# Kernel optimization log

Hardware: AMD Instinct MI355X
Metric: run time of the kernel (lower is better)

## Reference

```python
import jax, jax.numpy as jnp
import numpy as np

N = 100000
E = 640000
WIDTH = 128
NUM_FEATURES = 64


def _linear_relu(h, W, b):
    # LinearBlock with batch_norm=False, dropout=0.0 -> Linear + ReLU
    return jax.nn.relu(h @ W + b)


def setup_inputs() -> dict:
    key = jax.random.key(0)
    k = jax.random.split(key, 8)
    x = jax.random.normal(k[0], (N, WIDTH), dtype=jnp.float32)
    e = jax.random.randint(k[1], (2, E), 0, N, dtype=jnp.int32)
    e_feat = jax.random.normal(k[2], (E, NUM_FEATURES), dtype=jnp.float32)
    s_e = 1.0 / np.sqrt(WIDTH + NUM_FEATURES)
    s_m = 1.0 / np.sqrt(2 * WIDTH)
    W_edge = jax.random.uniform(k[3], (WIDTH + NUM_FEATURES, WIDTH), jnp.float32, -s_e, s_e)
    b_edge = jax.random.uniform(k[4], (WIDTH,), jnp.float32, -s_e, s_e)
    W_mlp = jax.random.uniform(k[5], (2 * WIDTH, WIDTH), jnp.float32, -s_m, s_m)
    b_mlp = jax.random.uniform(k[6], (WIDTH,), jnp.float32, -s_m, s_m)
    return {"x": x, "e": e, "e_feat": e_feat, "W_edge": W_edge, "b_edge": b_edge,
            "W_mlp": W_mlp, "b_mlp": b_mlp}


def reference(x, e, e_feat, W_edge, b_edge, W_mlp, b_mlp):
    src, dst = e[0], e[1]
    diffs = x[dst] - x[src]                                   # [E, width]
    ef = diffs + _linear_relu(jnp.concatenate([diffs, e_feat], axis=1), W_edge, b_edge)
    maxes = jax.ops.segment_max(ef, dst, num_segments=x.shape[0])  # [N, width]
    # torch_scatter.scatter_max leaves empty segments at 0
    maxes = jnp.where(jnp.isneginf(maxes), 0.0, maxes)
    return x + _linear_relu(jnp.concatenate([x, maxes], axis=1), W_mlp, b_mlp)
```

## Files before the change

### kernel.cpp

```cpp
#include <hip/hip_runtime.h>
#include <hip/hip_bf16.h>
#include <limits.h>

#define NNODES 100000
#define NEDGES 640000
#define WIDTH  128
#define NFEAT  64
#define KA     192
#define KA_PAD 200
#define KB     256
#define KB_PAD 264
#define MT     64
#define ST     130
#define NB_SCAN ((NNODES + 255) / 256)

typedef __attribute__((ext_vector_type(8))) short short8;
typedef __attribute__((ext_vector_type(4))) short short4v;
typedef __attribute__((ext_vector_type(4))) float floatx4;

__device__ __forceinline__ short f2bf_rne(float f) {
    unsigned u = __float_as_uint(f);
    unsigned r = u + 0x7fffu + ((u >> 16) & 1u);
    return (short)(r >> 16);
}
__device__ __forceinline__ short f2bf_t(float f) {
    return (short)(__float_as_uint(f) >> 16);
}
__device__ __forceinline__ float bf2f(short s) {
    return __uint_as_float(((unsigned)(unsigned short)s) << 16);
}
__device__ __forceinline__ unsigned encu(float f) {
    unsigned u = __float_as_uint(f);
    return (u & 0x80000000u) ? ~u : (u | 0x80000000u);
}
__device__ __forceinline__ float decu(unsigned e) {
    unsigned u = (e & 0x80000000u) ? (e ^ 0x80000000u) : ~e;
    return __uint_as_float(u);
}

__global__ __launch_bounds__(256) void prep_kernel(
    const float* __restrict__ W_edge, const float* __restrict__ W_mlp,
    short* __restrict__ We_t, short* __restrict__ Wm_t)
{
    int t = blockIdx.x * 256 + threadIdx.x;
    if (t < KA * WIDTH) {
        int k = t / WIDTH, n = t % WIDTH;
        We_t[n * KA + k] = f2bf_rne(W_edge[t]);
    } else if (t < (KA + KB) * WIDTH) {
        int j = t - KA * WIDTH;
        int k = j / WIDTH, n = j % WIDTH;
        Wm_t[n * KB + k] = f2bf_rne(W_mlp[j]);
    }
}

__global__ __launch_bounds__(256) void hist_kernel(
    const int* __restrict__ e, int* __restrict__ counts)
{
    int i = blockIdx.x * 256 + threadIdx.x;
    if (i < NEDGES) atomicAdd(&counts[e[NEDGES + i]], 1);
}

__global__ __launch_bounds__(256) void scanA_kernel(
    const int* __restrict__ counts, int* __restrict__ cursor, int* __restrict__ blockSum)
{
    __shared__ int s[256];
    int tid = threadIdx.x;
    int n = blockIdx.x * 256 + tid;
    int c = (n < NNODES) ? counts[n] : 0;
    s[tid] = c;
    __syncthreads();
    for (int off = 1; off < 256; off <<= 1) {
        int v = (tid >= off) ? s[tid - off] : 0;
        __syncthreads();
        s[tid] += v;
        __syncthreads();
    }
    if (n < NNODES) cursor[n] = s[tid] - c;
    if (tid == 255) blockSum[blockIdx.x] = s[255];
}

__global__ __launch_bounds__(512) void scanB_kernel(int* __restrict__ blockSum,
                                                    int* __restrict__ blockOff)
{
    __shared__ int s[512];
    int tid = threadIdx.x;
    int c = (tid < NB_SCAN) ? blockSum[tid] : 0;
    s[tid] = c;
    __syncthreads();
    for (int off = 1; off < 512; off <<= 1) {
        int v = (tid >= off) ? s[tid - off] : 0;
        __syncthreads();
        s[tid] += v;
        __syncthreads();
    }
    if (tid < NB_SCAN) blockOff[tid] = s[tid] - c;
}

__global__ __launch_bounds__(256) void scatter_kernel(
    const int* __restrict__ e, int* __restrict__ cursor,
    const int* __restrict__ blockOff,
    uint2* __restrict__ pSD, int* __restrict__ pEid)
{
    int i = blockIdx.x * 256 + threadIdx.x;
    if (i < NEDGES) {
        int s = e[i];
        int d = e[NEDGES + i];
        int p = atomicAdd(&cursor[d], 1) + blockOff[d >> 8];
        pSD[p] = make_uint2((unsigned)s, (unsigned)d);
        pEid[p] = i;
    }
}

__global__ __launch_bounds__(256, 4) void edge_kernel(
    const float* __restrict__ x, const float* __restrict__ e_feat,
    const short* __restrict__ We_t, const float* __restrict__ b_edge,
    const uint2* __restrict__ pSD, const int* __restrict__ pEid,
    unsigned* __restrict__ mEnc)
{
    __shared__ short sA[MT * KA_PAD];
    __shared__ float sBias[WIDTH];
    __shared__ int   sDst[MT];
    __shared__ int   sHeadRow[MT + 1];
    __shared__ int   sMeta[3];

    const int tid = threadIdx.x;
    if (tid < WIDTH) sBias[tid] = b_edge[tid];

    const int e0 = blockIdx.x * MT;
    const float4* xf4 = (const float4*)x;
    const float4* ef4 = (const float4*)e_feat;

    {
        int mq = tid >> 5, c = tid & 31;
        uint2 sd[8];
        #pragma unroll
        for (int j = 0; j < 8; ++j) sd[j] = pSD[e0 + mq + 8 * j];
        #pragma unroll
        for (int j = 0; j < 8; ++j) {
            int mm = mq + 8 * j;
            float4 xs = xf4[(size_t)sd[j].x * 32 + c];
            float4 xd = xf4[(size_t)sd[j].y * 32 + c];
            short4v df;
            df.x = f2bf_t(xd.x - xs.x);
            df.y = f2bf_t(xd.y - xs.y);
            df.z = f2bf_t(xd.z - xs.z);
            df.w = f2bf_t(xd.w - xs.w);
            *(short4v*)&sA[mm * KA_PAD + c * 4] = df;
            if (c == 0) sDst[mm] = (int)sd[j].y;
        }
        int mq2 = tid >> 4, c2 = tid & 15;
        int eid[4];
        #pragma unroll
        for (int j = 0; j < 4; ++j) eid[j] = pEid[e0 + mq2 + 16 * j];
        #pragma unroll
        for (int j = 0; j < 4; ++j) {
            int mm = mq2 + 16 * j;
            float4 fv = ef4[(size_t)eid[j] * 16 + c2];
            short4v sv;
            sv.x = f2bf_t(fv.x); sv.y = f2bf_t(fv.y);
            sv.z = f2bf_t(fv.z); sv.w = f2bf_t(fv.w);
            *(short4v*)&sA[mm * KA_PAD + WIDTH + c2 * 4] = sv;
        }
    }
    __syncthreads();

    if (tid < 64) {
        bool head = (tid == 0) || (sDst[tid] != sDst[tid - 1]);
        unsigned long long mask = __ballot(head);
        int rank = __popcll(mask & ((1ull << tid) - 1ull));
        if (head) sHeadRow[rank] = tid;
        if (tid == 0) {
            int nh = (int)__popcll(mask);
            sMeta[0] = nh;
            sHeadRow[nh] = MT;
            int prevSame = 0, nextSame = 0;
            if (e0 > 0)           prevSame = (pSD[e0 - 1].y  == (unsigned)sDst[0]);
            if (e0 + MT < NEDGES) nextSame = (pSD[e0 + MT].y == (unsigned)sDst[MT - 1]);
            sMeta[1] = prevSame; sMeta[2] = nextSame;
        }
    }

    const int wave = tid >> 6;
    const int lane = tid & 63;
    const int l15  = lane & 15;
    const int kq   = (lane >> 4) << 3;
    const int quad = lane >> 4;

    floatx4 acc[4][2];
    #pragma unroll
    for (int rt = 0; rt < 4; ++rt)
        #pragma unroll
        for (int ct = 0; ct < 2; ++ct)
            acc[rt][ct] = (floatx4){0.f, 0.f, 0.f, 0.f};

    #pragma unroll
    for (int kc = 0; kc < 6; ++kc) {
        int k0 = kc * 32 + kq;
        short8 a[4];
        #pragma unroll
        for (int rt = 0; rt < 4; ++rt)
            a[rt] = *(const short8*)&sA[(rt * 16 + l15) * KA_PAD + k0];
        short8 b[2];
        #pragma unroll
        for (int ct = 0; ct < 2; ++ct)
            b[ct] = *(const short8*)&We_t[(size_t)(wave * 32 + ct * 16 + l15) * KA + k0];
        #pragma unroll
        for (int rt = 0; rt < 4; ++rt)
            #pragma unroll
            for (int ct = 0; ct < 2; ++ct)
                acc[rt][ct] = __builtin_amdgcn_mfma_f32_16x16x32_bf16(a[rt], b[ct], acc[rt][ct], 0, 0, 0);
    }

    #pragma unroll
    for (int rt = 0; rt < 4; ++rt) {
        #pragma unroll
        for (int ct = 0; ct < 2; ++ct) {
            int col = wave * 32 + ct * 16 + l15;
            float bias = sBias[col];
            #pragma unroll
            for (int i = 0; i < 4; ++i) {
                int row = rt * 16 + quad * 4 + i;
                float v = acc[rt][ct][i] + bias;
                v = v > 0.f ? v : 0.f;
                acc[rt][ct][i] = v + bf2f(sA[row * KA_PAD + col]);
            }
        }
    }
    __syncthreads();

    short* sT = sA;
    #pragma unroll
    for (int rt = 0; rt < 4; ++rt) {
        #pragma unroll
        for (int ct = 0; ct < 2; ++ct) {
            int col = wave * 32 + ct * 16 + l15;
            #pragma unroll
            for (int i = 0; i < 4; ++i) {
                int row = rt * 16 + quad * 4 + i;
                sT[row * ST + col] = f2bf_t(acc[rt][ct][i]);
            }
        }
    }
    __syncthreads();

    const int nh = sMeta[0], prevSame = sMeta[1], nextSame = sMeta[2];
    const unsigned* sT32 = (const unsigned*)sT;
    for (int p = tid; p < nh * 64; p += 256) {
        int h = p >> 6, cp = p & 63;
        int r0 = sHeadRow[h], r1 = sHeadRow[h + 1];
        unsigned w = sT32[r0 * (ST / 2) + cp];
        float m0 = bf2f((short)(w & 0xffffu));
        float m1 = bf2f((short)(w >> 16));
        for (int r = r0 + 1; r < r1; ++r) {
            unsigned w2 = sT32[r * (ST / 2) + cp];
            m0 = fmaxf(m0, bf2f((short)(w2 & 0xffffu)));
            m1 = fmaxf(m1, bf2f((short)(w2 >> 16)));
        }
        int dst = sDst[r0];
        unsigned ev0 = encu(m0), ev1 = encu(m1);
        unsigned* dp = &mEnc[(size_t)dst * WIDTH + 2 * cp];
        bool atom = (h == 0 && prevSame) || (h == nh - 1 && nextSame);
        if (atom) { atomicMax(dp, ev0); atomicMax(dp + 1, ev1); }
        else      { *(uint2*)dp = make_uint2(ev0, ev1); }
    }
}

__global__ __launch_bounds__(256) void node_kernel(
    const float* __restrict__ x, const short* __restrict__ Wm_t,
    const float* __restrict__ b_mlp, float* __restrict__ out)
{
    __shared__ short sA[MT * KB_PAD];
    __shared__ float sBias[WIDTH];

    const int tid = threadIdx.x;
    if (tid < WIDTH) sBias[tid] = b_mlp[tid];

    const int n0 = blockIdx.x * MT;
    const float4* xf4 = (const float4*)x;
    const uint4* enc4 = (const uint4*)out;

    {
        int mq = tid >> 5, c = tid & 31;
        #pragma unroll
        for (int mm = mq; mm < MT; mm += 8) {
            int node = n0 + mm;
            if (node >= NNODES) node = NNODES - 1;
            float4 xv = xf4[(size_t)node * 32 + c];
            short4v sx;
            sx.x = f2bf_rne(xv.x); sx.y = f2bf_rne(xv.y);
            sx.z = f2bf_rne(xv.z); sx.w = f2bf_rne(xv.w);
            *(short4v*)&sA[mm * KB_PAD + c * 4] = sx;
            uint4 ev = enc4[(size_t)node * 32 + c];
            short4v sm;
            sm.x = f2bf_rne(ev.x == 0u ? 0.f : decu(ev.x));
            sm.y = f2bf_rne(ev.y == 0u ? 0.f : decu(ev.y));
            sm.z = f2bf_rne(ev.z == 0u ? 0.f : decu(ev.z));
            sm.w = f2bf_rne(ev.w == 0u ? 0.f : decu(ev.w));
            *(short4v*)&sA[mm * KB_PAD + WIDTH + c * 4] = sm;
        }
    }
    __syncthreads();

    const int wave = tid >> 6;
    const int lane = tid & 63;
    const int l15  = lane & 15;
    const int kq   = (lane >> 4) << 3;
    const int quad = lane >> 4;

    floatx4 acc[4][2];
    #pragma unroll
    for (int rt = 0; rt < 4; ++rt)
        #pragma unroll
        for (int ct = 0; ct < 2; ++ct)
            acc[rt][ct] = (floatx4){0.f, 0.f, 0.f, 0.f};

    #pragma unroll
    for (int kc = 0; kc < 8; ++kc) {
        int k0 = kc * 32 + kq;
        short8 a[4];
        #pragma unroll
        for (int rt = 0; rt < 4; ++rt)
            a[rt] = *(const short8*)&sA[(rt * 16 + l15) * KB_PAD + k0];
        short8 b[2];
        #pragma unroll
        for (int ct = 0; ct < 2; ++ct)
            b[ct] = *(const short8*)&Wm_t[(size_t)(wave * 32 + ct * 16 + l15) * KB + k0];
        #pragma unroll
        for (int rt = 0; rt < 4; ++rt)
            #pragma unroll
            for (int ct = 0; ct < 2; ++ct)
                acc[rt][ct] = __builtin_amdgcn_mfma_f32_16x16x32_bf16(a[rt], b[ct], acc[rt][ct], 0, 0, 0);
    }

    #pragma unroll
    for (int rt = 0; rt < 4; ++rt) {
        #pragma unroll
        for (int ct = 0; ct < 2; ++ct) {
            int col = wave * 32 + ct * 16 + l15;
            float bias = sBias[col];
            #pragma unroll
            for (int i = 0; i < 4; ++i) {
                int row = rt * 16 + quad * 4 + i;
                int node = n0 + row;
                if (node < NNODES) {
                    float v = acc[rt][ct][i] + bias;
                    v = v > 0.f ? v : 0.f;
                    out[(size_t)node * WIDTH + col] = x[(size_t)node * WIDTH + col] + v;
                }
            }
        }
    }
}

extern "C" void kernel_launch(void* const* d_in, const int* in_sizes, int n_in,
                              void* d_out, int out_size, void* d_ws, size_t ws_size,
                              hipStream_t stream) {
    const float* x      = (const float*)d_in[0];
    const int*   e      = (const int*)d_in[1];
    const float* e_feat = (const float*)d_in[2];
    const float* W_edge = (const float*)d_in[3];
    const float* b_edge = (const float*)d_in[4];
    const float* W_mlp  = (const float*)d_in[5];
    const float* b_mlp  = (const float*)d_in[6];
    float*    out  = (float*)d_out;
    unsigned* mEnc = (unsigned*)d_out;

    short* We_t = (short*)d_ws;
    short* Wm_t = We_t + (size_t)KA * WIDTH;
    int* base     = (int*)((char*)d_ws + 114688);
    uint2* pSD    = (uint2*)base;
    int* pEid     = (int*)(base + 2 * NEDGES);
    int* counts   = pEid + NEDGES;
    int* cursor   = counts + NNODES;
    int* blockSum = cursor + NNODES;
    int* blockOff = blockSum + NB_SCAN;

    hipMemsetAsync(d_out, 0, (size_t)NNODES * WIDTH * 4, stream);
    hipMemsetAsync(counts, 0, (size_t)NNODES * 4, stream);
    prep_kernel<<<((KA + KB) * WIDTH + 255) / 256, 256, 0, stream>>>(W_edge, W_mlp, We_t, Wm_t);
    hist_kernel<<<(NEDGES + 255) / 256, 256, 0, stream>>>(e, counts);
    scanA_kernel<<<NB_SCAN, 256, 0, stream>>>(counts, cursor, blockSum);
    scanB_kernel<<<1, 512, 0, stream>>>(blockSum, blockOff);
    scatter_kernel<<<(NEDGES + 255) / 256, 256, 0, stream>>>(e, cursor, blockOff, pSD, pEid);
    edge_kernel<<<NEDGES / MT, 256, 0, stream>>>(x, e_feat, We_t, b_edge, pSD, pEid, mEnc);
    node_kernel<<<(NNODES + MT - 1) / MT, 256, 0, stream>>>(x, Wm_t, b_mlp, out);
}
```

Measured before the change: 500.4 us.

## Batch edge gathers, transpose segment-max tile, swizzle blocks, fuse prep/hist kernels

Several changes land at once in the edge kernel. Gather loads for x and e_feat are issued in batches before conversion to raise memory-level parallelism, and the occupancy hint goes from 4 to 6 blocks. The LDS staging tile is transposed to column-major with packed 4-element stores, and each thread now reduces one column. Block indices are swizzled across the edge tiles, and the weight-prep kernel is fused with the histogram kernel to drop a launch. The added register pressure under the higher occupancy bound could cause spills.

```diff
diff --git a/kernel.cpp b/kernel.cpp
--- a/kernel.cpp
+++ b/kernel.cpp
@@ -7,12 +7,14 @@
 #define WIDTH  128
 #define NFEAT  64
 #define KA     192
-#define KA_PAD 200
+#define KA_PAD 196
 #define KB     256
 #define KB_PAD 264
 #define MT     64
-#define ST     130
+#define STC    68
 #define NB_SCAN ((NNODES + 255) / 256)
+#define NB_HIST ((NEDGES + 255) / 256)
+#define NB_PREP (((KA + KB) * WIDTH + 255) / 256)
 
 typedef __attribute__((ext_vector_type(8))) short short8;
 typedef __attribute__((ext_vector_type(4))) short short4v;
@@ -38,26 +40,26 @@
     return __uint_as_float(u);
 }
 
-__global__ __launch_bounds__(256) void prep_kernel(
+__global__ __launch_bounds__(256) void prep_hist_kernel(
+    const int* __restrict__ e, int* __restrict__ counts,
     const float* __restrict__ W_edge, const float* __restrict__ W_mlp,
     short* __restrict__ We_t, short* __restrict__ Wm_t)
 {
-    int t = blockIdx.x * 256 + threadIdx.x;
-    if (t < KA * WIDTH) {
-        int k = t / WIDTH, n = t % WIDTH;
-        We_t[n * KA + k] = f2bf_rne(W_edge[t]);
-    } else if (t < (KA + KB) * WIDTH) {
-        int j = t - KA * WIDTH;
-        int k = j / WIDTH, n = j % WIDTH;
-        Wm_t[n * KB + k] = f2bf_rne(W_mlp[j]);
-    }
-}
-
-__global__ __launch_bounds__(256) void hist_kernel(
-    const int* __restrict__ e, int* __restrict__ counts)
-{
-    int i = blockIdx.x * 256 + threadIdx.x;
-    if (i < NEDGES) atomicAdd(&counts[e[NEDGES + i]], 1);
+    int b = blockIdx.x;
+    if (b < NB_HIST) {
+        int i = b * 256 + threadIdx.x;
+        if (i < NEDGES) atomicAdd(&counts[e[NEDGES + i]], 1);
+    } else {
+        int t = (b - NB_HIST) * 256 + threadIdx.x;
+        if (t < KA * WIDTH) {
+            int k = t / WIDTH, n = t % WIDTH;
+            We_t[n * KA + k] = f2bf_rne(W_edge[t]);
+        } else if (t < (KA + KB) * WIDTH) {
+            int j = t - KA * WIDTH;
+            int k = j / WIDTH, n = j % WIDTH;
+            Wm_t[n * KB + k] = f2bf_rne(W_mlp[j]);
+        }
+    }
 }
 
 __global__ __launch_bounds__(256) void scanA_kernel(
@@ -111,13 +113,13 @@
     }
 }
 
-__global__ __launch_bounds__(256, 4) void edge_kernel(
+__global__ __launch_bounds__(256, 6) void edge_kernel(
     const float* __restrict__ x, const float* __restrict__ e_feat,
     const short* __restrict__ We_t, const float* __restrict__ b_edge,
     const uint2* __restrict__ pSD, const int* __restrict__ pEid,
     unsigned* __restrict__ mEnc)
 {
-    __shared__ short sA[MT * KA_PAD];
+    __shared__ __align__(16) short sA[MT * KA_PAD];
     __shared__ float sBias[WIDTH];
     __shared__ int   sDst[MT];
     __shared__ int   sHeadRow[MT + 1];
@@ -126,7 +128,10 @@
     const int tid = threadIdx.x;
     if (tid < WIDTH) sBias[tid] = b_edge[tid];
 
-    const int e0 = blockIdx.x * MT;
+    const int bid = blockIdx.x;
+    const int btile = (bid & 7) * (NEDGES / MT / 8) + (bid >> 3);
+    const int e0 = btile * MT;
+
     const float4* xf4 = (const float4*)x;
     const float4* ef4 = (const float4*)e_feat;
 
@@ -135,30 +140,56 @@
         uint2 sd[8];
         #pragma unroll
         for (int j = 0; j < 8; ++j) sd[j] = pSD[e0 + mq + 8 * j];
-        #pragma unroll
-        for (int j = 0; j < 8; ++j) {
-            int mm = mq + 8 * j;
-            float4 xs = xf4[(size_t)sd[j].x * 32 + c];
-            float4 xd = xf4[(size_t)sd[j].y * 32 + c];
-            short4v df;
-            df.x = f2bf_t(xd.x - xs.x);
-            df.y = f2bf_t(xd.y - xs.y);
-            df.z = f2bf_t(xd.z - xs.z);
-            df.w = f2bf_t(xd.w - xs.w);
-            *(short4v*)&sA[mm * KA_PAD + c * 4] = df;
-            if (c == 0) sDst[mm] = (int)sd[j].y;
-        }
         int mq2 = tid >> 4, c2 = tid & 15;
         int eid[4];
         #pragma unroll
         for (int j = 0; j < 4; ++j) eid[j] = pEid[e0 + mq2 + 16 * j];
+
+        float4 xsA[4], xdA[4];
+        #pragma unroll
+        for (int j = 0; j < 4; ++j) {
+            xsA[j] = xf4[(size_t)sd[j].x * 32 + c];
+            xdA[j] = xf4[(size_t)sd[j].y * 32 + c];
+        }
+        float4 xsB[4], xdB[4];
+        #pragma unroll
+        for (int j = 0; j < 4; ++j) {
+            xsB[j] = xf4[(size_t)sd[4 + j].x * 32 + c];
+            xdB[j] = xf4[(size_t)sd[4 + j].y * 32 + c];
+        }
+        if (c == 0) {
+            #pragma unroll
+            for (int j = 0; j < 8; ++j) sDst[mq + 8 * j] = (int)sd[j].y;
+        }
+        #pragma unroll
+        for (int j = 0; j < 4; ++j) {
+            int mm = mq + 8 * j;
+            short4v df;
+            df.x = f2bf_t(xdA[j].x - xsA[j].x);
+            df.y = f2bf_t(xdA[j].y - xsA[j].y);
+            df.z = f2bf_t(xdA[j].z - xsA[j].z);
+            df.w = f2bf_t(xdA[j].w - xsA[j].w);
+            *(short4v*)&sA[mm * KA_PAD + c * 4] = df;
+        }
+        float4 fv[4];
+        #pragma unroll
+        for (int j = 0; j < 4; ++j) fv[j] = ef4[(size_t)eid[j] * 16 + c2];
+        #pragma unroll
+        for (int j = 0; j < 4; ++j) {
+            int mm = mq + 8 * (4 + j);
+            short4v df;
+            df.x = f2bf_t(xdB[j].x - xsB[j].x);
+            df.y = f2bf_t(xdB[j].y - xsB[j].y);
+            df.z = f2bf_t(xdB[j].z - xsB[j].z);
+            df.w = f2bf_t(xdB[j].w - xsB[j].w);
+            *(short4v*)&sA[mm * KA_PAD + c * 4] = df;
+        }
         #pragma unroll
         for (int j = 0; j < 4; ++j) {
             int mm = mq2 + 16 * j;
-            float4 fv = ef4[(size_t)eid[j] * 16 + c2];
             short4v sv;
-            sv.x = f2bf_t(fv.x); sv.y = f2bf_t(fv.y);
-            sv.z = f2bf_t(fv.z); sv.w = f2bf_t(fv.w);
+            sv.x = f2bf_t(fv[j].x); sv.y = f2bf_t(fv[j].y);
+            sv.z = f2bf_t(fv[j].z); sv.w = f2bf_t(fv[j].w);
             *(short4v*)&sA[mm * KA_PAD + WIDTH + c2 * 4] = sv;
         }
     }
@@ -234,34 +265,37 @@
         #pragma unroll
         for (int ct = 0; ct < 2; ++ct) {
             int col = wave * 32 + ct * 16 + l15;
-            #pragma unroll
-            for (int i = 0; i < 4; ++i) {
-                int row = rt * 16 + quad * 4 + i;
-                sT[row * ST + col] = f2bf_t(acc[rt][ct][i]);
-            }
+            short4v pk;
+            pk.x = f2bf_t(acc[rt][ct][0]);
+            pk.y = f2bf_t(acc[rt][ct][1]);
+            pk.z = f2bf_t(acc[rt][ct][2]);
+            pk.w = f2bf_t(acc[rt][ct][3]);
+            *(short4v*)&sT[col * STC + rt * 16 + quad * 4] = pk;
         }
     }
     __syncthreads();
 
     const int nh = sMeta[0], prevSame = sMeta[1], nextSame = sMeta[2];
     const unsigned* sT32 = (const unsigned*)sT;
-    for (int p = tid; p < nh * 64; p += 256) {
-        int h = p >> 6, cp = p & 63;
+    for (int p = tid; p < (nh << 7); p += 256) {
+        int h = p >> 7, c = p & 127;
         int r0 = sHeadRow[h], r1 = sHeadRow[h + 1];
-        unsigned w = sT32[r0 * (ST / 2) + cp];
-        float m0 = bf2f((short)(w & 0xffffu));
-        float m1 = bf2f((short)(w >> 16));
-        for (int r = r0 + 1; r < r1; ++r) {
-            unsigned w2 = sT32[r * (ST / 2) + cp];
-            m0 = fmaxf(m0, bf2f((short)(w2 & 0xffffu)));
-            m1 = fmaxf(m1, bf2f((short)(w2 >> 16)));
+        const unsigned* colp = sT32 + c * (STC / 2);
+        int w0 = r0 >> 1, w1 = (r1 - 1) >> 1;
+        float m = -3.4e38f;
+        for (int w = w0; w <= w1; ++w) {
+            unsigned u = colp[w];
+            float flo = bf2f((short)(u & 0xffffu));
+            float fhi = bf2f((short)(u >> 16));
+            if (2 * w >= r0)    m = fmaxf(m, flo);
+            if (2 * w + 1 < r1) m = fmaxf(m, fhi);
         }
         int dst = sDst[r0];
-        unsigned ev0 = encu(m0), ev1 = encu(m1);
-        unsigned* dp = &mEnc[(size_t)dst * WIDTH + 2 * cp];
+        unsigned ev = encu(m);
+        unsigned* dp = &mEnc[(size_t)dst * WIDTH + c];
         bool atom = (h == 0 && prevSame) || (h == nh - 1 && nextSame);
-        if (atom) { atomicMax(dp, ev0); atomicMax(dp + 1, ev1); }
-        else      { *(uint2*)dp = make_uint2(ev0, ev1); }
+        if (atom) atomicMax(dp, ev);
+        else      *dp = ev;
     }
 }
 
@@ -377,8 +411,7 @@
 
     hipMemsetAsync(d_out, 0, (size_t)NNODES * WIDTH * 4, stream);
     hipMemsetAsync(counts, 0, (size_t)NNODES * 4, stream);
-    prep_kernel<<<((KA + KB) * WIDTH + 255) / 256, 256, 0, stream>>>(W_edge, W_mlp, We_t, Wm_t);
-    hist_kernel<<<(NEDGES + 255) / 256, 256, 0, stream>>>(e, counts);
+    prep_hist_kernel<<<NB_HIST + NB_PREP, 256, 0, stream>>>(e, counts, W_edge, W_mlp, We_t, Wm_t);
     scanA_kernel<<<NB_SCAN, 256, 0, stream>>>(counts, cursor, blockSum);
     scanB_kernel<<<1, 512, 0, stream>>>(blockSum, blockOff);
     scatter_kernel<<<(NEDGES + 255) / 256, 256, 0, stream>>>(e, cursor, blockOff, pSD, pEid);
```

Result: slower. 536.2 us (+7.1%).
